# Optimization experiments

Measured on AMD Instinct MI355X. Metric: run time of the kernel, lower is better.

Reference implementation:

```python
import jax, jax.numpy as jnp
import numpy as np
import math

B, L, D, H = 2, 2048, 1024, 16
DK = D // H


def setup_inputs() -> dict:
    key = jax.random.key(0)
    ks = jax.random.split(key, 11)
    s = 1.0 / math.sqrt(D)
    inp = {
        "query": jax.random.normal(ks[0], (B, L, D), jnp.float32),
        "key": jax.random.normal(ks[1], (B, L, D), jnp.float32),
        "value": jax.random.normal(ks[2], (B, L, D), jnp.float32),
        # mask == True (==1) means masked-out; causal mask over future positions
        "mask": jnp.triu(jnp.ones((L, L), dtype=bool), k=1),
        "Wq": jax.random.normal(ks[3], (D, D), jnp.float32) * s,
        "bq": jnp.zeros((D,), jnp.float32),
        "Wk": jax.random.normal(ks[4], (D, D), jnp.float32) * s,
        "bk": jnp.zeros((D,), jnp.float32),
        "Wv": jax.random.normal(ks[5], (D, D), jnp.float32) * s,
        "bv": jnp.zeros((D,), jnp.float32),
        "Wo": jax.random.normal(ks[6], (D, D), jnp.float32) * s,
        "bo": jnp.zeros((D,), jnp.float32),
    }
    return inp


def reference(query, key, value, mask, Wq, bq, Wk, bk, Wv, bv, Wo, bo):
    # Linear projections, then split heads: [B, L, D] -> [B, H, L, DK]
    def proj(x, W, b):
        return (x @ W.T + b).reshape(B, -1, H, DK).transpose(0, 2, 1, 3)

    Q = proj(query, Wq, bq)
    K = proj(key, Wk, bk)
    V = proj(value, Wv, bv)

    scale = 1.0 / math.sqrt(DK)
    scores = jnp.einsum("bhqd,bhkd->bhqk", Q, K) * scale  # [B,H,Lq,Lk]
    scores = jnp.where(mask, -jnp.inf, scores)
    attn = jax.nn.softmax(scores, axis=-1)  # dropout p=0 (eval mode)
    out = jnp.einsum("bhqk,bhkd->bhqd", attn, V)
    out = out.transpose(0, 2, 1, 3).reshape(B, -1, D)  # merge heads
    return out @ Wo.T + bo
```

## Files before the change

### kernel.cpp

```cpp
#include <hip/hip_runtime.h>
#include <hip/hip_bf16.h>
#include <math.h>

#define NL 2048
#define ND 1024

typedef __attribute__((ext_vector_type(8))) __bf16 bf16x8;
typedef __attribute__((ext_vector_type(4))) float f32x4;
typedef __attribute__((ext_vector_type(16))) float f32x16;
typedef __attribute__((ext_vector_type(4))) short short4v;
typedef __attribute__((ext_vector_type(2))) unsigned uint2v;
typedef __attribute__((ext_vector_type(4))) unsigned uint4v;

__device__ __forceinline__ short f2bf(float f) {
    union { float f; unsigned u; } v; v.f = f;
    unsigned u = v.u;
    u += 0x7FFF + ((u >> 16) & 1);
    return (short)(u >> 16);
}

__device__ __forceinline__ unsigned cvtpk2(float lo, float hi) {
    unsigned r;
    asm("v_cvt_pk_bf16_f32 %0, %1, %2" : "=v"(r) : "v"(lo), "v"(hi));
    return r;
}

__device__ __forceinline__ void gload16(const short* g, short* l) {
    __builtin_amdgcn_global_load_lds(
        (const __attribute__((address_space(1))) void*)g,
        (__attribute__((address_space(3))) void*)l, 16, 0, 0);
}

__global__ __launch_bounds__(256) void cvt3(const float* __restrict__ a,
                                            const float* __restrict__ b,
                                            const float* __restrict__ c,
                                            short* __restrict__ da,
                                            short* __restrict__ db,
                                            short* __restrict__ dc, int per) {
    const float* src = blockIdx.y == 0 ? a : blockIdx.y == 1 ? b : c;
    short* d = blockIdx.y == 0 ? da : blockIdx.y == 1 ? db : dc;
    int i = (blockIdx.x * 256 + threadIdx.x) * 8;
    if (i < per) {
        f32x4 v0 = *(const f32x4*)&src[i];
        f32x4 v1 = *(const f32x4*)&src[i + 4];
        uint4v u = { cvtpk2(v0[0], v0[1]), cvtpk2(v0[2], v0[3]),
                     cvtpk2(v1[0], v1[1]), cvtpk2(v1[2], v1[3]) };
        *(uint4v*)&d[i] = u;
    }
}

__device__ __forceinline__ void gemm_core(const short* gA, const short* gB,
                                          short (*As)[4096], short (*Bs)[4096],
                                          int w, int wr, int wc, int lr, int lc,
                                          f32x4 acc[4][4]) {
    gload16(gA,         &As[0][w * 512]);
    gload16(gA + 65536, &As[0][w * 512 + 2048]);
    gload16(gB,         &Bs[0][w * 512]);
    gload16(gB + 65536, &Bs[0][w * 512 + 2048]);
    gload16(gA + 32,         &As[1][w * 512]);
    gload16(gA + 65536 + 32, &As[1][w * 512 + 2048]);
    gload16(gB + 32,         &Bs[1][w * 512]);
    gload16(gB + 65536 + 32, &Bs[1][w * 512 + 2048]);

    for (int t = 0; t < 30; ++t) {
        const int ws_ = (t + 2) & 3, rd = t & 3;
        const int k2 = (t + 2) * 32;
        gload16(gA + k2,         &As[ws_][w * 512]);
        gload16(gA + 65536 + k2, &As[ws_][w * 512 + 2048]);
        gload16(gB + k2,         &Bs[ws_][w * 512]);
        gload16(gB + 65536 + k2, &Bs[ws_][w * 512 + 2048]);
        asm volatile("s_waitcnt vmcnt(8)" ::: "memory");
        __builtin_amdgcn_s_barrier();
        asm volatile("" ::: "memory");

        bf16x8 a[4], b[4];
        #pragma unroll
        for (int mt = 0; mt < 4; ++mt)
            a[mt] = *(const bf16x8*)&As[rd][(wr * 64 + mt * 16 + lc) * 32 + lr * 8];
        #pragma unroll
        for (int nt = 0; nt < 4; ++nt)
            b[nt] = *(const bf16x8*)&Bs[rd][(wc * 64 + nt * 16 + lc) * 32 + lr * 8];
        __builtin_amdgcn_s_setprio(1);
        #pragma unroll
        for (int mt = 0; mt < 4; ++mt)
            #pragma unroll
            for (int nt = 0; nt < 4; ++nt)
                acc[mt][nt] = __builtin_amdgcn_mfma_f32_16x16x32_bf16(
                    a[mt], b[nt], acc[mt][nt], 0, 0, 0);
        __builtin_amdgcn_s_setprio(0);
    }
    #pragma unroll
    for (int pt = 0; pt < 2; ++pt) {
        if (pt == 0) asm volatile("s_waitcnt vmcnt(4)" ::: "memory");
        else         asm volatile("s_waitcnt vmcnt(0)" ::: "memory");
        __builtin_amdgcn_s_barrier();
        asm volatile("" ::: "memory");
        const int rd = 2 + pt;
        bf16x8 a[4], b[4];
        #pragma unroll
        for (int mt = 0; mt < 4; ++mt)
            a[mt] = *(const bf16x8*)&As[rd][(wr * 64 + mt * 16 + lc) * 32 + lr * 8];
        #pragma unroll
        for (int nt = 0; nt < 4; ++nt)
            b[nt] = *(const bf16x8*)&Bs[rd][(wc * 64 + nt * 16 + lc) * 32 + lr * 8];
        #pragma unroll
        for (int mt = 0; mt < 4; ++mt)
            #pragma unroll
            for (int nt = 0; nt < 4; ++nt)
                acc[mt][nt] = __builtin_amdgcn_mfma_f32_16x16x32_bf16(
                    a[mt], b[nt], acc[mt][nt], 0, 0, 0);
    }
}

__global__ __launch_bounds__(256) void gemm_qk(
    const short* __restrict__ Xqb, const short* __restrict__ Xkb,
    const short* __restrict__ Wqb, const short* __restrict__ Wkb,
    const float* __restrict__ bq, const float* __restrict__ bk,
    short* __restrict__ oq, short* __restrict__ ok) {
    __shared__ alignas(16) short As[4][4096];
    __shared__ alignas(16) short Bs[4][4096];

    const int bid  = blockIdx.x;
    const int xcd  = bid & 7, slot = bid >> 3;
    const int panel = xcd * 8 + (slot >> 3);
    const int zz   = panel >> 5;
    const int m0   = (panel & 31) * 128;
    const int n0   = (slot & 7) * 128;

    const short* Ab = zz ? Xkb : Xqb;
    const short* Wb = zz ? Wkb : Wqb;
    const float* bi = zz ? bk : bq;
    short* outp     = zz ? ok : oq;
    const float scl = zz ? 1.0f : 0.125f * 1.44269504088896f;

    const int tid = threadIdx.x, lane = tid & 63, w = tid >> 6;
    const int wr = w >> 1, wc = w & 1, lr = lane >> 4, lc = lane & 15;

    const short* gA = &Ab[(m0 + w * 16 + (lane >> 2)) * 1024 + (lane & 3) * 8];
    const short* gB = &Wb[(n0 + w * 16 + (lane >> 2)) * 1024 + (lane & 3) * 8];

    f32x4 acc[4][4] = {};
    gemm_core(gA, gB, As, Bs, w, wr, wc, lr, lc, acc);

    #pragma unroll
    for (int mt = 0; mt < 4; ++mt)
        #pragma unroll
        for (int nt = 0; nt < 4; ++nt)
            #pragma unroll
            for (int r = 0; r < 4; ++r) {
                int grow = m0 + wr * 64 + mt * 16 + lr * 4 + r;
                int gcol = n0 + wc * 64 + nt * 16 + lc;
                float val = (acc[mt][nt][r] + bi[gcol]) * scl;
                int bh = (grow >> 11) * 16 + (gcol >> 6);
                int q  = grow & 2047;
                int dk = gcol & 63;
                size_t addr = (size_t)bh * 131072 + (size_t)(q >> 5) * 2048 +
                              (dk >> 4) * 512 + ((dk >> 3) & 1) * 256 +
                              (q & 31) * 8 + (dk & 7);
                outp[addr] = f2bf(val);
            }
}

__global__ __launch_bounds__(256) void gemm_v(
    const short* __restrict__ Xvb, const short* __restrict__ Wvb,
    const float* __restrict__ bv, short* __restrict__ ov) {
    __shared__ alignas(16) short As[4][4096];
    __shared__ alignas(16) short Bs[4][4096];

    const int bid = blockIdx.x;
    const int xcd = bid & 7, slot = bid >> 3;
    const int m0  = (xcd * 4 + (slot >> 3)) * 128;
    const int n0  = (slot & 7) * 128;

    const int tid = threadIdx.x, lane = tid & 63, w = tid >> 6;
    const int wr = w >> 1, wc = w & 1, lr = lane >> 4, lc = lane & 15;

    const short* gA = &Xvb[(m0 + w * 16 + (lane >> 2)) * 1024 + (lane & 3) * 8];
    const short* gB = &Wvb[(n0 + w * 16 + (lane >> 2)) * 1024 + (lane & 3) * 8];

    f32x4 acc[4][4] = {};
    gemm_core(gA, gB, As, Bs, w, wr, wc, lr, lc, acc);

    #pragma unroll
    for (int mt = 0; mt < 4; ++mt)
        #pragma unroll
        for (int nt = 0; nt < 4; ++nt)
            #pragma unroll
            for (int r = 0; r < 4; ++r) {
                int grow = m0 + wr * 64 + mt * 16 + lr * 4 + r;
                int gcol = n0 + wc * 64 + nt * 16 + lc;
                float val = acc[mt][nt][r] + bv[gcol];
                int bh = (grow >> 11) * 16 + (gcol >> 6);
                int q  = grow & 2047;
                int dk = gcol & 63;
                size_t addr = (size_t)bh * 131072 + (size_t)(q >> 6) * 4096 +
                              ((q >> 4) & 3) * 1024 + (dk >> 5) * 512 +
                              ((q >> 3) & 1) * 256 + (dk & 31) * 8 + (q & 7);
                outp_store: outp_store_dummy:;
                ov[addr] = f2bf(val);
            }
}

__global__ __launch_bounds__(256) void gemm_out(const short* __restrict__ Abf,
                                                const short* __restrict__ Wob,
                                                const float* __restrict__ bo,
                                                float* __restrict__ out) {
    __shared__ alignas(16) short As[4][4096];
    __shared__ alignas(16) short Bs[4][4096];

    const int bid = blockIdx.x;
    const int xcd = bid & 7, slot = bid >> 3;
    const int m0  = (xcd * 4 + (slot >> 3)) * 128;
    const int n0  = (slot & 7) * 128;

    const int tid = threadIdx.x, lane = tid & 63, w = tid >> 6;
    const int wr = w >> 1, wc = w & 1, lr = lane >> 4, lc = lane & 15;

    const short* gA = &Abf[(m0 + w * 16 + (lane >> 2)) * 1024 + (lane & 3) * 8];
    const short* gB = &Wob[(n0 + w * 16 + (lane >> 2)) * 1024 + (lane & 3) * 8];

    f32x4 acc[4][4] = {};
    gemm_core(gA, gB, As, Bs, w, wr, wc, lr, lc, acc);

    #pragma unroll
    for (int mt = 0; mt < 4; ++mt)
        #pragma unroll
        for (int nt = 0; nt < 4; ++nt)
            #pragma unroll
            for (int r = 0; r < 4; ++r) {
                int grow = m0 + wr * 64 + mt * 16 + lr * 4 + r;
                int gcol = n0 + wc * 64 + nt * 16 + lc;
                out[grow * 1024 + gcol] = acc[mt][nt][r] + bo[gcol];
            }
}

__global__ __launch_bounds__(128, 3) void flash_attn(const short* __restrict__ Q,
                                                     const short* __restrict__ K,
                                                     const short* __restrict__ Vt,
                                                     short* __restrict__ AO) {
    __shared__ float mrg[64][49];

    const int tid  = threadIdx.x;
    const int lane = tid & 63;
    const int w    = tid >> 6;
    const int ql   = lane & 31;
    const int hi   = lane >> 5;

    const int bid  = blockIdx.x;
    const int xcd  = bid & 7;
    const int idx  = bid >> 3;
    const int bh   = xcd * 4 + (idx & 3);
    const int t    = 63 - (idx >> 2);
    const int q0   = t * 32;
    const int qa   = q0 + ql;
    const int nkb  = (t >> 1) + 1;
    const int nkb2 = nkb >> 1;
    const int kb_lo = w == 0 ? 0 : nkb2;
    const int kb_hi = w == 0 ? nkb2 : nkb;

    const short* Qp = Q  + (size_t)bh * 131072 + (size_t)t * 2048 + lane * 8;
    const short* Kp = K  + (size_t)bh * 131072 + lane * 8;
    const short* Vp = Vt + (size_t)bh * 131072 + lane * 8;

    bf16x8 qf[4];
    #pragma unroll
    for (int ks = 0; ks < 4; ++ks)
        qf[ks] = *(const bf16x8*)&Qp[ks * 512];

    f32x16 ot0 = {}, ot1 = {}, lacc = {};

    for (int kb = kb_lo; kb < kb_hi; ++kb) {
        bf16x8 kf[8];
        #pragma unroll
        for (int ks = 0; ks < 4; ++ks) {
            kf[2 * ks]     = *(const bf16x8*)&Kp[(size_t)(2 * kb) * 2048 + ks * 512];
            kf[2 * ks + 1] = *(const bf16x8*)&Kp[(size_t)(2 * kb + 1) * 2048 + ks * 512];
        }

        f32x16 st0 = {}, st1 = {};
        __builtin_amdgcn_s_setprio(1);
        #pragma unroll
        for (int ks = 0; ks < 4; ++ks) {
            st0 = __builtin_amdgcn_mfma_f32_32x32x16_bf16(kf[2 * ks],     qf[ks], st0, 0, 0, 0);
            st1 = __builtin_amdgcn_mfma_f32_32x32x16_bf16(kf[2 * ks + 1], qf[ks], st1, 0, 0, 0);
        }
        __builtin_amdgcn_s_setprio(0);

        bf16x8 vf[8];
        #pragma unroll
        for (int ks = 0; ks < 4; ++ks) {
            vf[2 * ks]     = *(const bf16x8*)&Vp[(size_t)kb * 4096 + ks * 1024];
            vf[2 * ks + 1] = *(const bf16x8*)&Vp[(size_t)kb * 4096 + ks * 1024 + 512];
        }

        if (kb == nkb - 1) {
            const int kv0 = kb * 64;
            #pragma unroll
            for (int r = 0; r < 16; ++r) {
                const int cr = (r & 3) + 8 * (r >> 2) + 4 * hi;
                if (kv0 + cr > qa)      st0[r] = -3.0e38f;
                if (kv0 + 32 + cr > qa) st1[r] = -3.0e38f;
            }
        }

        #pragma unroll
        for (int r = 0; r < 16; ++r) {
            st0[r] = exp2f(st0[r]);
            st1[r] = exp2f(st1[r]);
            lacc[r] += st0[r] + st1[r];
        }

        bf16x8 pf[4];
        #pragma unroll
        for (int blk = 0; blk < 2; ++blk) {
            const f32x16 s = blk ? st1 : st0;
            #pragma unroll
            for (int pks = 0; pks < 2; ++pks) {
                const int b = pks * 8;
                unsigned xa = cvtpk2(s[b + 0], s[b + 1]);
                unsigned xb = cvtpk2(s[b + 2], s[b + 3]);
                unsigned ya = cvtpk2(s[b + 4], s[b + 5]);
                unsigned yb = cvtpk2(s[b + 6], s[b + 7]);
                uint2v s0 = __builtin_amdgcn_permlane32_swap(xa, ya, false, false);
                uint2v s1 = __builtin_amdgcn_permlane32_swap(xb, yb, false, false);
                union { unsigned u[4]; bf16x8 v; } pu;
                pu.u[0] = s0[0]; pu.u[1] = s1[0]; pu.u[2] = s0[1]; pu.u[3] = s1[1];
                pf[blk * 2 + pks] = pu.v;
            }
        }

        __builtin_amdgcn_s_setprio(1);
        #pragma unroll
        for (int ks = 0; ks < 4; ++ks) {
            ot0 = __builtin_amdgcn_mfma_f32_32x32x16_bf16(vf[2 * ks],     pf[ks], ot0, 0, 0, 0);
            ot1 = __builtin_amdgcn_mfma_f32_32x32x16_bf16(vf[2 * ks + 1], pf[ks], ot1, 0, 0, 0);
        }
        __builtin_amdgcn_s_setprio(0);
    }

    if (w == 0) {
        #pragma unroll
        for (int r = 0; r < 16; ++r) {
            mrg[lane][r]      = ot0[r];
            mrg[lane][16 + r] = ot1[r];
            mrg[lane][32 + r] = lacc[r];
        }
    }
    __syncthreads();
    if (w == 1) {
        #pragma unroll
        for (int r = 0; r < 16; ++r) {
            ot0[r]  += mrg[lane][r];
            ot1[r]  += mrg[lane][16 + r];
            lacc[r] += mrg[lane][32 + r];
        }
        float sm[16];
        #pragma unroll
        for (int r = 0; r < 16; ++r) sm[r] = lacc[r];
        #pragma unroll
        for (int s = 8; s > 0; s >>= 1)
            #pragma unroll
            for (int i = 0; i < s; ++i) sm[i] += sm[i + s];
        const float l = sm[0] + __shfl_xor(sm[0], 32);
        const float inv = 1.f / l;

        const int b_ = bh >> 4, h_ = bh & 15;
        short* aoRow = AO + ((size_t)(b_ * NL + qa)) * ND + h_ * 64;
        #pragma unroll
        for (int db = 0; db < 2; ++db) {
            const f32x16 o = db ? ot1 : ot0;
            #pragma unroll
            for (int g = 0; g < 4; ++g) {
                short4v sv;
                #pragma unroll
                for (int i = 0; i < 4; ++i) sv[i] = f2bf(o[g * 4 + i] * inv);
                *(short4v*)&aoRow[db * 32 + g * 8 + 4 * hi] = sv;
            }
        }
    }
}

extern "C" void kernel_launch(void* const* d_in, const int* in_sizes, int n_in,
                              void* d_out, int out_size, void* d_ws, size_t ws_size,
                              hipStream_t stream) {
    const float* query = (const float*)d_in[0];
    const float* key   = (const float*)d_in[1];
    const float* value = (const float*)d_in[2];
    const float* Wq = (const float*)d_in[4];
    const float* bq = (const float*)d_in[5];
    const float* Wk = (const float*)d_in[6];
    const float* bk = (const float*)d_in[7];
    const float* Wv = (const float*)d_in[8];
    const float* bv = (const float*)d_in[9];
    const float* Wo = (const float*)d_in[10];
    const float* bo = (const float*)d_in[11];

    short* ws    = (short*)d_ws;
    short* dob   = (short*)d_out;
    short* q_ws  = ws;
    short* k_ws  = ws + (4 << 20);
    short* xq    = ws + (8 << 20);
    short* vt_ws = ws + (8 << 20);
    short* wbf   = ws + (12 << 20);
    short* ao_ws = ws + (12 << 20);
    short* wobf  = ws;
    short* xk    = dob;
    short* xv    = dob + (4 << 20);

    cvt3<<<dim3(512, 3), 256, 0, stream>>>(Wq, Wk, Wv,
                                           wbf, wbf + (1 << 20), wbf + (2 << 20), 1 << 20);
    cvt3<<<dim3(2048, 3), 256, 0, stream>>>(query, key, value, xq, xk, xv, 4 << 20);
    gemm_qk<<<dim3(512), 256, 0, stream>>>(xq, xk, wbf, wbf + (1 << 20),
                                           bq, bk, q_ws, k_ws);
    gemm_v<<<dim3(256), 256, 0, stream>>>(xv, wbf + (2 << 20), bv, vt_ws);
    flash_attn<<<dim3(2048), dim3(128), 0, stream>>>(q_ws, k_ws, vt_ws, ao_ws);
    cvt3<<<dim3(512, 1), 256, 0, stream>>>(Wo, Wo, Wo, wobf, wobf, wobf, 1 << 20);
    gemm_out<<<dim3(256), 256, 0, stream>>>(ao_ws, wobf, bo, (float*)d_out);
}
```

Baseline: 133.8 us.

## Split flash-attn KV range over four waves, fuse conversion launches, hoist V loads

Flash attention now uses 256 threads per block, so four waves each take a quarter of the causal KV blocks instead of two waves taking halves. Partial outputs and row sums are combined with a two-stage tree reduction through a larger shared buffer. V fragment loads are issued before the QK MFMAs so their latency overlaps the score compute. The input and weight bf16 conversions are merged into one launch to cut launch overhead. The cost is more reduction work, an extra barrier, and higher register pressure from holding V fragments earlier, with the old launch_bounds occupancy hint removed.

```diff
diff --git a/kernel.cpp b/kernel.cpp
--- a/kernel.cpp
+++ b/kernel.cpp
@@ -31,22 +31,43 @@
         (__attribute__((address_space(3))) void*)l, 16, 0, 0);
 }
 
-__global__ __launch_bounds__(256) void cvt3(const float* __restrict__ a,
-                                            const float* __restrict__ b,
-                                            const float* __restrict__ c,
-                                            short* __restrict__ da,
-                                            short* __restrict__ db,
-                                            short* __restrict__ dc, int per) {
-    const float* src = blockIdx.y == 0 ? a : blockIdx.y == 1 ? b : c;
-    short* d = blockIdx.y == 0 ? da : blockIdx.y == 1 ? db : dc;
-    int i = (blockIdx.x * 256 + threadIdx.x) * 8;
-    if (i < per) {
-        f32x4 v0 = *(const f32x4*)&src[i];
-        f32x4 v1 = *(const f32x4*)&src[i + 4];
-        uint4v u = { cvtpk2(v0[0], v0[1]), cvtpk2(v0[2], v0[3]),
-                     cvtpk2(v1[0], v1[1]), cvtpk2(v1[2], v1[3]) };
-        *(uint4v*)&d[i] = u;
-    }
+__global__ __launch_bounds__(256) void cvt_all(
+    const float* __restrict__ q, const float* __restrict__ k, const float* __restrict__ v,
+    const float* __restrict__ wq, const float* __restrict__ wk, const float* __restrict__ wv,
+    short* __restrict__ xq, short* __restrict__ xk, short* __restrict__ xv,
+    short* __restrict__ wbf) {
+    const int bid = blockIdx.x;
+    const float* src;
+    short* dst;
+    int blk;
+    if (bid < 6144) {
+        const int t = bid >> 11;
+        src = t == 0 ? q : t == 1 ? k : v;
+        dst = t == 0 ? xq : t == 1 ? xk : xv;
+        blk = bid & 2047;
+    } else {
+        const int b2 = bid - 6144;
+        const int t = b2 >> 9;
+        src = t == 0 ? wq : t == 1 ? wk : wv;
+        dst = wbf + (size_t)t * (1 << 20);
+        blk = b2 & 511;
+    }
+    const int i = blk * 2048 + threadIdx.x * 8;
+    f32x4 v0 = *(const f32x4*)&src[i];
+    f32x4 v1 = *(const f32x4*)&src[i + 4];
+    uint4v u = { cvtpk2(v0[0], v0[1]), cvtpk2(v0[2], v0[3]),
+                 cvtpk2(v1[0], v1[1]), cvtpk2(v1[2], v1[3]) };
+    *(uint4v*)&dst[i] = u;
+}
+
+__global__ __launch_bounds__(256) void cvt1(const float* __restrict__ src,
+                                            short* __restrict__ dst) {
+    const int i = blockIdx.x * 2048 + threadIdx.x * 8;
+    f32x4 v0 = *(const f32x4*)&src[i];
+    f32x4 v1 = *(const f32x4*)&src[i + 4];
+    uint4v u = { cvtpk2(v0[0], v0[1]), cvtpk2(v0[2], v0[3]),
+                 cvtpk2(v1[0], v1[1]), cvtpk2(v1[2], v1[3]) };
+    *(uint4v*)&dst[i] = u;
 }
 
 __device__ __forceinline__ void gemm_core(const short* gA, const short* gB,
@@ -196,7 +217,6 @@
                 size_t addr = (size_t)bh * 131072 + (size_t)(q >> 6) * 4096 +
                               ((q >> 4) & 3) * 1024 + (dk >> 5) * 512 +
                               ((q >> 3) & 1) * 256 + (dk & 31) * 8 + (q & 7);
-                outp_store: outp_store_dummy:;
                 ov[addr] = f2bf(val);
             }
 }
@@ -234,11 +254,11 @@
             }
 }
 
-__global__ __launch_bounds__(128, 3) void flash_attn(const short* __restrict__ Q,
-                                                     const short* __restrict__ K,
-                                                     const short* __restrict__ Vt,
-                                                     short* __restrict__ AO) {
-    __shared__ float mrg[64][49];
+__global__ __launch_bounds__(256) void flash_attn(const short* __restrict__ Q,
+                                                  const short* __restrict__ K,
+                                                  const short* __restrict__ Vt,
+                                                  short* __restrict__ AO) {
+    __shared__ float mrg[2][64][49];
 
     const int tid  = threadIdx.x;
     const int lane = tid & 63;
@@ -254,9 +274,8 @@
     const int q0   = t * 32;
     const int qa   = q0 + ql;
     const int nkb  = (t >> 1) + 1;
-    const int nkb2 = nkb >> 1;
-    const int kb_lo = w == 0 ? 0 : nkb2;
-    const int kb_hi = w == 0 ? nkb2 : nkb;
+    const int kb_lo = (w * nkb) >> 2;
+    const int kb_hi = ((w + 1) * nkb) >> 2;
 
     const short* Qp = Q  + (size_t)bh * 131072 + (size_t)t * 2048 + lane * 8;
     const short* Kp = K  + (size_t)bh * 131072 + lane * 8;
@@ -276,6 +295,12 @@
             kf[2 * ks]     = *(const bf16x8*)&Kp[(size_t)(2 * kb) * 2048 + ks * 512];
             kf[2 * ks + 1] = *(const bf16x8*)&Kp[(size_t)(2 * kb + 1) * 2048 + ks * 512];
         }
+        bf16x8 vf[8];
+        #pragma unroll
+        for (int ks = 0; ks < 4; ++ks) {
+            vf[2 * ks]     = *(const bf16x8*)&Vp[(size_t)kb * 4096 + ks * 1024];
+            vf[2 * ks + 1] = *(const bf16x8*)&Vp[(size_t)kb * 4096 + ks * 1024 + 512];
+        }
 
         f32x16 st0 = {}, st1 = {};
         __builtin_amdgcn_s_setprio(1);
@@ -285,13 +310,6 @@
             st1 = __builtin_amdgcn_mfma_f32_32x32x16_bf16(kf[2 * ks + 1], qf[ks], st1, 0, 0, 0);
         }
         __builtin_amdgcn_s_setprio(0);
-
-        bf16x8 vf[8];
-        #pragma unroll
-        for (int ks = 0; ks < 4; ++ks) {
-            vf[2 * ks]     = *(const bf16x8*)&Vp[(size_t)kb * 4096 + ks * 1024];
-            vf[2 * ks + 1] = *(const bf16x8*)&Vp[(size_t)kb * 4096 + ks * 1024 + 512];
-        }
 
         if (kb == nkb - 1) {
             const int kv0 = kb * 64;
@@ -338,21 +356,34 @@
         __builtin_amdgcn_s_setprio(0);
     }
 
+    if (w >= 2) {
+        float* m = &mrg[w - 2][lane][0];
+        #pragma unroll
+        for (int r = 0; r < 16; ++r) {
+            m[r] = ot0[r]; m[16 + r] = ot1[r]; m[32 + r] = lacc[r];
+        }
+    }
+    __syncthreads();
+    if (w < 2) {
+        const float* m = &mrg[w][lane][0];
+        #pragma unroll
+        for (int r = 0; r < 16; ++r) {
+            ot0[r] += m[r]; ot1[r] += m[16 + r]; lacc[r] += m[32 + r];
+        }
+    }
+    if (w == 1) {
+        float* m = &mrg[1][lane][0];
+        #pragma unroll
+        for (int r = 0; r < 16; ++r) {
+            m[r] = ot0[r]; m[16 + r] = ot1[r]; m[32 + r] = lacc[r];
+        }
+    }
+    __syncthreads();
     if (w == 0) {
+        const float* m = &mrg[1][lane][0];
         #pragma unroll
         for (int r = 0; r < 16; ++r) {
-            mrg[lane][r]      = ot0[r];
-            mrg[lane][16 + r] = ot1[r];
-            mrg[lane][32 + r] = lacc[r];
-        }
-    }
-    __syncthreads();
-    if (w == 1) {
-        #pragma unroll
-        for (int r = 0; r < 16; ++r) {
-            ot0[r]  += mrg[lane][r];
-            ot1[r]  += mrg[lane][16 + r];
-            lacc[r] += mrg[lane][32 + r];
+            ot0[r] += m[r]; ot1[r] += m[16 + r]; lacc[r] += m[32 + r];
         }
         float sm[16];
         #pragma unroll
@@ -407,13 +438,12 @@
     short* xk    = dob;
     short* xv    = dob + (4 << 20);
 
-    cvt3<<<dim3(512, 3), 256, 0, stream>>>(Wq, Wk, Wv,
-                                           wbf, wbf + (1 << 20), wbf + (2 << 20), 1 << 20);
-    cvt3<<<dim3(2048, 3), 256, 0, stream>>>(query, key, value, xq, xk, xv, 4 << 20);
+    cvt_all<<<dim3(7680), 256, 0, stream>>>(query, key, value, Wq, Wk, Wv,
+                                            xq, xk, xv, wbf);
     gemm_qk<<<dim3(512), 256, 0, stream>>>(xq, xk, wbf, wbf + (1 << 20),
                                            bq, bk, q_ws, k_ws);
     gemm_v<<<dim3(256), 256, 0, stream>>>(xv, wbf + (2 << 20), bv, vt_ws);
-    flash_attn<<<dim3(2048), dim3(128), 0, stream>>>(q_ws, k_ws, vt_ws, ao_ws);
-    cvt3<<<dim3(512, 1), 256, 0, stream>>>(Wo, Wo, Wo, wobf, wobf, wobf, 1 << 20);
+    flash_attn<<<dim3(2048), dim3(256), 0, stream>>>(q_ws, k_ws, vt_ws, ao_ws);
+    cvt1<<<dim3(512), 256, 0, stream>>>(Wo, wobf);
     gemm_out<<<dim3(256), 256, 0, stream>>>(ao_ws, wobf, bo, (float*)d_out);
 }
```

After: 134.6 us. No clear change (+0.6%).
